# Optimization experiments

Measured on AMD Instinct MI355X. Metric: run time of the kernel, lower is better.

The kernel has to match this reference:

```python
import jax, jax.numpy as jnp
import numpy as np

N_OBJ = 8192        # total proposals across the batch
N_REL = 32768       # total relation pairs across the batch
HID = 512           # CONTEXT_HIDDEN_DIM
POOL = 4096         # CONTEXT_POOLING_DIM (== MLP_HEAD_DIM -> no up_dim)
N_OBJ_CLS = 151     # VG object classes
N_REL_CLS = 51      # VG relation classes


def setup_inputs() -> dict:
    key = jax.random.key(0)
    ks = jax.random.split(key, 8)
    edge_ctx = jax.random.normal(ks[0], (N_OBJ, HID), jnp.float32)
    union_features = jax.random.normal(ks[1], (N_REL, POOL), jnp.float32)
    rel_pair_idx = jax.random.randint(ks[2], (N_REL, 2), 0, N_OBJ)
    obj_preds = jax.random.randint(ks[3], (N_OBJ,), 0, N_OBJ_CLS)
    # layer_init(post_emb, 10 * (1/hidden)**0.5, normal=True)
    W_post_emb = jax.random.normal(ks[4], (HID, 2 * HID), jnp.float32) * (10.0 * (1.0 / HID) ** 0.5)
    b_post_emb = jnp.zeros((2 * HID,), jnp.float32)
    # xavier inits for post_cat / ctx_compress
    W_post_cat = jax.random.normal(ks[5], (2 * HID, POOL), jnp.float32) * np.float32(np.sqrt(2.0 / (2 * HID + POOL)))
    b_post_cat = jnp.zeros((POOL,), jnp.float32)
    W_ctx = jax.random.normal(ks[6], (POOL, N_REL_CLS), jnp.float32) * np.float32(np.sqrt(2.0 / (POOL + N_REL_CLS)))
    b_ctx = jnp.zeros((N_REL_CLS,), jnp.float32)
    # frequency-bias embedding table: rows indexed by head_cls*151 + tail_cls
    freq_table = jax.random.normal(ks[7], (N_OBJ_CLS * N_OBJ_CLS, N_REL_CLS), jnp.float32) * 0.01
    return {
        "edge_ctx": edge_ctx, "union_features": union_features,
        "rel_pair_idx": rel_pair_idx, "obj_preds": obj_preds,
        "W_post_emb": W_post_emb, "b_post_emb": b_post_emb,
        "W_post_cat": W_post_cat, "b_post_cat": b_post_cat,
        "W_ctx": W_ctx, "b_ctx": b_ctx, "freq_table": freq_table,
    }


def reference(edge_ctx, union_features, rel_pair_idx, obj_preds,
              W_post_emb, b_post_emb, W_post_cat, b_post_cat,
              W_ctx, b_ctx, freq_table):
    # edge_rep = relu(post_emb(edge_ctx)).view(N, 2, hidden)
    edge_rep = jax.nn.relu(edge_ctx @ W_post_emb + b_post_emb).reshape(-1, 2, HID)
    head_rep = edge_rep[:, 0]  # [N_obj, HID]
    tail_rep = edge_rep[:, 1]
    # edge-wise gather of head/tail node reps (global indices == per-image split+index)
    h = head_rep[rel_pair_idx[:, 0]]  # [N_rel, HID]
    t = tail_rep[rel_pair_idx[:, 1]]
    prod_rep = jnp.concatenate([h, t], axis=-1) @ W_post_cat + b_post_cat  # [N_rel, POOL]
    ctx_dists = (prod_rep * union_features) @ W_ctx + b_ctx               # [N_rel, 51]
    # frequency bias: index_with_labels(pair_pred)
    pair_idx = obj_preds[rel_pair_idx[:, 0]] * N_OBJ_CLS + obj_preds[rel_pair_idx[:, 1]]
    frq_dists = freq_table[pair_idx]  # [N_rel, 51]
    return ctx_dists + frq_dists
```

## Files before the change

kernel.cpp:

```cpp
#include <hip/hip_runtime.h>
#include <hip/hip_bf16.h>

#define N_OBJ 8192
#define N_REL 32768
#define HID   512
#define POOL  4096
#define NOC   151
#define NRC   51

typedef __bf16 bf16_t;
typedef __attribute__((ext_vector_type(8))) __bf16 bf16x8;
typedef __attribute__((ext_vector_type(4))) __bf16 bf16x4;
typedef __attribute__((ext_vector_type(4))) float f32x4;

__device__ __forceinline__ void async_copy16(const void* g, void* l) {
    __builtin_amdgcn_global_load_lds((__attribute__((address_space(1))) void*)g,
                                     (__attribute__((address_space(3))) void*)l,
                                     16, 0, 0);
}


__global__ void convert_bf16_kernel(const float* __restrict__ in,
                                    bf16_t* __restrict__ out, int n4) {
    int i = blockIdx.x * blockDim.x + threadIdx.x;
    int stride = gridDim.x * blockDim.x;
    for (; i < n4; i += stride) {
        float4 v = ((const float4*)in)[i];
        bf16x4 o;
        o[0] = (bf16_t)v.x; o[1] = (bf16_t)v.y; o[2] = (bf16_t)v.z; o[3] = (bf16_t)v.w;
        ((bf16x4*)out)[i] = o;
    }
}

__global__ void transpose_bf16_kernel(const float* __restrict__ in,
                                      bf16_t* __restrict__ out,
                                      int K, int C, int Cpad) {
    __shared__ float tile[32][33];
    int cb = blockIdx.x * 32, kb = blockIdx.y * 32;
    int tx = threadIdx.x, ty = threadIdx.y;
    #pragma unroll
    for (int i = 0; i < 32; i += 8) {
        int k = kb + ty + i, c = cb + tx;
        float v = (k < K && c < C) ? in[(size_t)k * C + c] : 0.0f;
        tile[ty + i][tx] = v;
    }
    __syncthreads();
    #pragma unroll
    for (int i = 0; i < 32; i += 8) {
        int c = cb + ty + i, k = kb + tx;
        if (c < Cpad && k < K) out[(size_t)c * K + k] = (bf16_t)tile[tx][ty + i];
    }
}


__global__ __launch_bounds__(256, 2) void gemm1_kernel(
    const bf16_t* __restrict__ A,
    const bf16_t* __restrict__ Bt,
    const float* __restrict__ bias,
    bf16_t* __restrict__ C)
{
    __shared__ __align__(16) bf16_t As[128 * 64];
    __shared__ __align__(16) bf16_t Bs[128 * 64];
    const int tid = threadIdx.x;
    const int w = tid >> 6, lane = tid & 63;
    const int m0 = blockIdx.x * 128, n0 = blockIdx.y * 128;
    const int lrow = tid >> 3, lcs = tid & 7;
    const int wm = w & 1, wn = w >> 1;
    const int quad = lane >> 4, l16 = lane & 15;
    f32x4 acc[4][4] = {};

    for (int kt = 0; kt < HID / 64; ++kt) {
        const int k0 = kt * 64;
        #pragma unroll
        for (int j = 0; j < 4; ++j) {
            int ml = j * 32 + lrow;
            int cg = lcs ^ (ml & 7);
            async_copy16(A + (size_t)(m0 + ml) * HID + k0 + cg * 8, &As[ml * 64 + lcs * 8]);
        }
        #pragma unroll
        for (int j = 0; j < 4; ++j) {
            int nl = j * 32 + lrow;
            int cg = lcs ^ (nl & 7);
            async_copy16(Bt + (size_t)(n0 + nl) * HID + k0 + cg * 8, &Bs[nl * 64 + lcs * 8]);
        }
        __syncthreads();
        #pragma unroll
        for (int kb = 0; kb < 2; ++kb) {
            bf16x8 a[4], b[4];
            #pragma unroll
            for (int i = 0; i < 4; ++i) {
                int m = wm * 64 + i * 16 + l16;
                int ch = (kb * 4 + quad) ^ (m & 7);
                a[i] = *(const bf16x8*)&As[m * 64 + ch * 8];
            }
            #pragma unroll
            for (int i = 0; i < 4; ++i) {
                int n = wn * 64 + i * 16 + l16;
                int ch = (kb * 4 + quad) ^ (n & 7);
                b[i] = *(const bf16x8*)&Bs[n * 64 + ch * 8];
            }
            #pragma unroll
            for (int i = 0; i < 4; ++i)
                #pragma unroll
                for (int jj = 0; jj < 4; ++jj)
                    acc[i][jj] = __builtin_amdgcn_mfma_f32_16x16x32_bf16(a[i], b[jj], acc[i][jj], 0, 0, 0);
        }
        __syncthreads();
    }
    #pragma unroll
    for (int i = 0; i < 4; ++i) {
        int rbase = m0 + wm * 64 + i * 16 + quad * 4;
        #pragma unroll
        for (int jj = 0; jj < 4; ++jj) {
            int c = n0 + wn * 64 + jj * 16 + l16;
            float bv = bias[c];
            #pragma unroll
            for (int rr = 0; rr < 4; ++rr) {
                float v = acc[i][jj][rr] + bv;
                v = fmaxf(v, 0.0f);
                C[(size_t)(rbase + rr) * 1024 + c] = (bf16_t)v;
            }
        }
    }
}


__global__ __launch_bounds__(256, 2) void gemm_half_kernel(
    const bf16_t* __restrict__ C1,
    const bf16_t* __restrict__ Wcat_t,
    bf16_t* __restrict__ HWb,
    bf16_t* __restrict__ TWb)
{
    __shared__ __align__(16) bf16_t As[128 * 64];
    __shared__ __align__(16) bf16_t Bs[128 * 64];
    const int tid = threadIdx.x;
    const int w = tid >> 6, lane = tid & 63;
    const int m0 = blockIdx.x * 128, n0 = blockIdx.y * 128;
    const int koff = blockIdx.z * 512;
    bf16_t* const Cout = blockIdx.z ? TWb : HWb;
    const int lrow = tid >> 3, lcs = tid & 7;
    const int wm = w & 1, wn = w >> 1;
    const int quad = lane >> 4, l16 = lane & 15;
    f32x4 acc[4][4] = {};

    for (int kt = 0; kt < 8; ++kt) {
        const int k0 = koff + kt * 64;
        #pragma unroll
        for (int j = 0; j < 4; ++j) {
            int ml = j * 32 + lrow;
            int cg = lcs ^ (ml & 7);
            async_copy16(C1 + (size_t)(m0 + ml) * 1024 + k0 + cg * 8, &As[ml * 64 + lcs * 8]);
        }
        #pragma unroll
        for (int j = 0; j < 4; ++j) {
            int nl = j * 32 + lrow;
            int cg = lcs ^ (nl & 7);
            async_copy16(Wcat_t + (size_t)(n0 + nl) * 1024 + k0 + cg * 8, &Bs[nl * 64 + lcs * 8]);
        }
        __syncthreads();
        #pragma unroll
        for (int kb = 0; kb < 2; ++kb) {
            bf16x8 a[4], b[4];
            #pragma unroll
            for (int i = 0; i < 4; ++i) {
                int m = wm * 64 + i * 16 + l16;
                int ch = (kb * 4 + quad) ^ (m & 7);
                a[i] = *(const bf16x8*)&As[m * 64 + ch * 8];
            }
            #pragma unroll
            for (int i = 0; i < 4; ++i) {
                int n = wn * 64 + i * 16 + l16;
                int ch = (kb * 4 + quad) ^ (n & 7);
                b[i] = *(const bf16x8*)&Bs[n * 64 + ch * 8];
            }
            #pragma unroll
            for (int i = 0; i < 4; ++i)
                #pragma unroll
                for (int jj = 0; jj < 4; ++jj)
                    acc[i][jj] = __builtin_amdgcn_mfma_f32_16x16x32_bf16(a[i], b[jj], acc[i][jj], 0, 0, 0);
        }
        __syncthreads();
    }
    #pragma unroll
    for (int i = 0; i < 4; ++i) {
        int rbase = m0 + wm * 64 + i * 16 + quad * 4;
        #pragma unroll
        for (int jj = 0; jj < 4; ++jj) {
            int c = n0 + wn * 64 + jj * 16 + l16;
            #pragma unroll
            for (int rr = 0; rr < 4; ++rr)
                Cout[(size_t)(rbase + rr) * POOL + c] = (bf16_t)acc[i][jj][rr];
        }
    }
}


__global__ __launch_bounds__(512, 2) void rel_fused_kernel(
    const bf16_t* __restrict__ HWb,
    const bf16_t* __restrict__ TWb,
    const bf16_t* __restrict__ Wctx_t,
    const int* __restrict__ rel,
    const int* __restrict__ obj,
    const float* __restrict__ b_cat,
    const float* __restrict__ b_ctx,
    const float* __restrict__ freq,
    const float* __restrict__ uni,
    float* __restrict__ out)
{
    __shared__ __align__(16) bf16_t Ss[2][64 * 128];
    const int tid = threadIdx.x;
    const int w = tid >> 6, lane = tid & 63;
    const int quad = lane >> 4, l16 = lane & 15;
    const int wm = w & 1, wn = w >> 1;
    const int lr = tid >> 3, hc = tid & 7;
    const int m0 = blockIdx.x * 64;

    const int myrow = m0 + lr;
    const int gi0 = rel[2 * myrow], gi1 = rel[2 * myrow + 1];
    const bf16_t* hwrow = HWb + (size_t)gi0 * POOL;
    const bf16_t* twrow = TWb + (size_t)gi1 * POOL;
    const float*  urow  = uni + (size_t)myrow * POOL;

    f32x4 acc2[2] = {};

    auto scale_pass = [&](int kc, bf16_t* S) {
        const int cbase = kc * 128 + hc * 16;
        #pragma unroll
        for (int cg = 0; cg < 2; ++cg) {
            const int cc = cbase + cg * 8;
            bf16x8 hw = *(const bf16x8*)&hwrow[cc];
            bf16x8 tw = *(const bf16x8*)&twrow[cc];
            float4 u0 = *(const float4*)&urow[cc];
            float4 u1 = *(const float4*)&urow[cc + 4];
            float4 b0 = *(const float4*)&b_cat[cc];
            float4 b1 = *(const float4*)&b_cat[cc + 4];
            bf16x8 s;
            s[0] = (bf16_t)(((float)hw[0] + (float)tw[0] + b0.x) * u0.x);
            s[1] = (bf16_t)(((float)hw[1] + (float)tw[1] + b0.y) * u0.y);
            s[2] = (bf16_t)(((float)hw[2] + (float)tw[2] + b0.z) * u0.z);
            s[3] = (bf16_t)(((float)hw[3] + (float)tw[3] + b0.w) * u0.w);
            s[4] = (bf16_t)(((float)hw[4] + (float)tw[4] + b1.x) * u1.x);
            s[5] = (bf16_t)(((float)hw[5] + (float)tw[5] + b1.y) * u1.y);
            s[6] = (bf16_t)(((float)hw[6] + (float)tw[6] + b1.z) * u1.z);
            s[7] = (bf16_t)(((float)hw[7] + (float)tw[7] + b1.w) * u1.w);
            const int colc = hc * 2 + cg;
            *(bf16x8*)&S[lr * 128 + ((colc ^ (lr & 15)) << 3)] = s;
        }
    };
    auto mma_pass = [&](int kc, const bf16_t* S) {
        #pragma unroll
        for (int kb = 0; kb < 4; ++kb) {
            bf16x8 a2[2], b2;
            #pragma unroll
            for (int i = 0; i < 2; ++i) {
                int m = wm * 32 + i * 16 + l16;
                a2[i] = *(const bf16x8*)&S[m * 128 + (((kb * 4 + quad) ^ (m & 15)) << 3)];
            }
            int c = wn * 16 + l16;
            b2 = *(const bf16x8*)&Wctx_t[(size_t)c * POOL + kc * 128 + kb * 32 + quad * 8];
            #pragma unroll
            for (int i = 0; i < 2; ++i)
                acc2[i] = __builtin_amdgcn_mfma_f32_16x16x32_bf16(a2[i], b2, acc2[i], 0, 0, 0);
        }
    };

    scale_pass(0, Ss[0]);
    __syncthreads();
    for (int kc = 0; kc < 32; ++kc) {
        bf16_t* Scur = Ss[kc & 1];
        bf16_t* Snxt = Ss[(kc & 1) ^ 1];
        if (kc < 31) scale_pass(kc + 1, Snxt);
        mma_pass(kc, Scur);
        __syncthreads();
    }

    #pragma unroll
    for (int i = 0; i < 2; ++i) {
        #pragma unroll
        for (int rr = 0; rr < 4; ++rr) {
            int row = m0 + wm * 32 + i * 16 + quad * 4 + rr;
            int c = wn * 16 + l16;
            if (c < NRC) {
                int pid = obj[rel[2 * row]] * NOC + obj[rel[2 * row + 1]];
                out[(size_t)row * NRC + c] =
                    acc2[i][rr] + b_ctx[c] + freq[(size_t)pid * NRC + c];
            }
        }
    }
}


extern "C" void kernel_launch(void* const* d_in, const int* in_sizes, int n_in,
                              void* d_out, int out_size, void* d_ws, size_t ws_size,
                              hipStream_t stream) {
    const float* edge_ctx = (const float*)d_in[0];
    const float* uni      = (const float*)d_in[1];
    const int*   rel      = (const int*)d_in[2];
    const int*   obj      = (const int*)d_in[3];
    const float* W_emb    = (const float*)d_in[4];
    const float* b_emb    = (const float*)d_in[5];
    const float* W_cat    = (const float*)d_in[6];
    const float* b_cat    = (const float*)d_in[7];
    const float* W_ctx    = (const float*)d_in[8];
    const float* b_ctx    = (const float*)d_in[9];
    const float* freq     = (const float*)d_in[10];
    float* out = (float*)d_out;

    char* p = (char*)d_ws;
    bf16_t* C1     = (bf16_t*)p; p += (size_t)N_OBJ * 1024 * 2;
    bf16_t* ecb    = (bf16_t*)p; p += (size_t)N_OBJ * HID * 2;
    bf16_t* Wemb_t = (bf16_t*)p; p += (size_t)1024 * HID * 2;
    bf16_t* Wcat_t = (bf16_t*)p; p += (size_t)POOL * 1024 * 2;
    bf16_t* Wctx_t = (bf16_t*)p; p += (size_t)64 * POOL * 2;
    bf16_t* HWb    = (bf16_t*)p; p += (size_t)N_OBJ * POOL * 2;
    bf16_t* TWb    = (bf16_t*)p; p += (size_t)N_OBJ * POOL * 2;

    convert_bf16_kernel<<<2048, 256, 0, stream>>>(edge_ctx, ecb, N_OBJ * HID / 4);
    transpose_bf16_kernel<<<dim3(1024 / 32, HID / 32), dim3(32, 8), 0, stream>>>(W_emb, Wemb_t, HID, 1024, 1024);
    transpose_bf16_kernel<<<dim3(POOL / 32, 1024 / 32), dim3(32, 8), 0, stream>>>(W_cat, Wcat_t, 1024, POOL, POOL);
    transpose_bf16_kernel<<<dim3(2, POOL / 32), dim3(32, 8), 0, stream>>>(W_ctx, Wctx_t, POOL, NRC, 64);

    gemm1_kernel<<<dim3(N_OBJ / 128, 1024 / 128), 256, 0, stream>>>(ecb, Wemb_t, b_emb, C1);
    gemm_half_kernel<<<dim3(N_OBJ / 128, POOL / 128, 2), 256, 0, stream>>>(C1, Wcat_t, HWb, TWb);
    rel_fused_kernel<<<N_REL / 64, 512, 0, stream>>>(HWb, TWb, Wctx_t, rel, obj,
                                                     b_cat, b_ctx, freq, uni, out);
}
```

Baseline: 897.0 us.

## Merge prep kernels into one launch and shrink rel tile to 16 rows

```diff
diff --git a/kernel.cpp b/kernel.cpp
--- a/kernel.cpp
+++ b/kernel.cpp
@@ -20,24 +20,33 @@
 }
 
 
-__global__ void convert_bf16_kernel(const float* __restrict__ in,
-                                    bf16_t* __restrict__ out, int n4) {
-    int i = blockIdx.x * blockDim.x + threadIdx.x;
-    int stride = gridDim.x * blockDim.x;
-    for (; i < n4; i += stride) {
-        float4 v = ((const float4*)in)[i];
-        bf16x4 o;
-        o[0] = (bf16_t)v.x; o[1] = (bf16_t)v.y; o[2] = (bf16_t)v.z; o[3] = (bf16_t)v.w;
-        ((bf16x4*)out)[i] = o;
-    }
-}
-
-__global__ void transpose_bf16_kernel(const float* __restrict__ in,
-                                      bf16_t* __restrict__ out,
-                                      int K, int C, int Cpad) {
+__global__ void prep_kernel(const float* __restrict__ W_emb, bf16_t* __restrict__ Wemb_t,
+                            const float* __restrict__ W_cat, bf16_t* __restrict__ Wcat_t,
+                            const float* __restrict__ W_ctx, bf16_t* __restrict__ Wctx_t,
+                            const float* __restrict__ ec,    bf16_t* __restrict__ ecb) {
+    const int bid = blockIdx.x;
+    if (bid >= 4864) {
+        const int tid = threadIdx.y * 32 + threadIdx.x;
+        int i = (bid - 4864) * 256 + tid;
+        const int n4 = N_OBJ * HID / 4;
+        const int stride = 2048 * 256;
+        for (; i < n4; i += stride) {
+            float4 v = ((const float4*)ec)[i];
+            bf16x4 o;
+            o[0] = (bf16_t)v.x; o[1] = (bf16_t)v.y; o[2] = (bf16_t)v.z; o[3] = (bf16_t)v.w;
+            ((bf16x4*)ecb)[i] = o;
+        }
+        return;
+    }
+    const float* in; bf16_t* outp; int K, C, Cpad, cb, kb;
+    if (bid < 512)       { in = W_emb; outp = Wemb_t; K = HID;  C = 1024; Cpad = 1024;
+                           cb = (bid & 31) << 5; kb = (bid >> 5) << 5; }
+    else if (bid < 4608) { int b = bid - 512;  in = W_cat; outp = Wcat_t; K = 1024; C = POOL; Cpad = POOL;
+                           cb = (b & 127) << 5; kb = (b >> 7) << 5; }
+    else                 { int b = bid - 4608; in = W_ctx; outp = Wctx_t; K = POOL; C = NRC;  Cpad = 64;
+                           cb = (b & 1) << 5;  kb = (b >> 1) << 5; }
     __shared__ float tile[32][33];
-    int cb = blockIdx.x * 32, kb = blockIdx.y * 32;
-    int tx = threadIdx.x, ty = threadIdx.y;
+    const int tx = threadIdx.x, ty = threadIdx.y;
     #pragma unroll
     for (int i = 0; i < 32; i += 8) {
         int k = kb + ty + i, c = cb + tx;
@@ -48,7 +57,7 @@
     #pragma unroll
     for (int i = 0; i < 32; i += 8) {
         int c = cb + ty + i, k = kb + tx;
-        if (c < Cpad && k < K) out[(size_t)c * K + k] = (bf16_t)tile[tx][ty + i];
+        if (c < Cpad && k < K) outp[(size_t)c * K + k] = (bf16_t)tile[tx][ty + i];
     }
 }
 
@@ -195,7 +204,7 @@
 }
 
 
-__global__ __launch_bounds__(512, 2) void rel_fused_kernel(
+__global__ __launch_bounds__(256, 6) void rel_fused_kernel(
     const bf16_t* __restrict__ HWb,
     const bf16_t* __restrict__ TWb,
     const bf16_t* __restrict__ Wctx_t,
@@ -207,13 +216,12 @@
     const float* __restrict__ uni,
     float* __restrict__ out)
 {
-    __shared__ __align__(16) bf16_t Ss[2][64 * 128];
+    __shared__ __align__(16) bf16_t Ss[2][16 * 128];
     const int tid = threadIdx.x;
     const int w = tid >> 6, lane = tid & 63;
     const int quad = lane >> 4, l16 = lane & 15;
-    const int wm = w & 1, wn = w >> 1;
-    const int lr = tid >> 3, hc = tid & 7;
-    const int m0 = blockIdx.x * 64;
+    const int lr = tid >> 4, hc = tid & 15;
+    const int m0 = blockIdx.x * 16;
 
     const int myrow = m0 + lr;
     const int gi0 = rel[2 * myrow], gi1 = rel[2 * myrow + 1];
@@ -221,46 +229,35 @@
     const bf16_t* twrow = TWb + (size_t)gi1 * POOL;
     const float*  urow  = uni + (size_t)myrow * POOL;
 
-    f32x4 acc2[2] = {};
+    f32x4 acc = {};
 
     auto scale_pass = [&](int kc, bf16_t* S) {
-        const int cbase = kc * 128 + hc * 16;
-        #pragma unroll
-        for (int cg = 0; cg < 2; ++cg) {
-            const int cc = cbase + cg * 8;
-            bf16x8 hw = *(const bf16x8*)&hwrow[cc];
-            bf16x8 tw = *(const bf16x8*)&twrow[cc];
-            float4 u0 = *(const float4*)&urow[cc];
-            float4 u1 = *(const float4*)&urow[cc + 4];
-            float4 b0 = *(const float4*)&b_cat[cc];
-            float4 b1 = *(const float4*)&b_cat[cc + 4];
-            bf16x8 s;
-            s[0] = (bf16_t)(((float)hw[0] + (float)tw[0] + b0.x) * u0.x);
-            s[1] = (bf16_t)(((float)hw[1] + (float)tw[1] + b0.y) * u0.y);
-            s[2] = (bf16_t)(((float)hw[2] + (float)tw[2] + b0.z) * u0.z);
-            s[3] = (bf16_t)(((float)hw[3] + (float)tw[3] + b0.w) * u0.w);
-            s[4] = (bf16_t)(((float)hw[4] + (float)tw[4] + b1.x) * u1.x);
-            s[5] = (bf16_t)(((float)hw[5] + (float)tw[5] + b1.y) * u1.y);
-            s[6] = (bf16_t)(((float)hw[6] + (float)tw[6] + b1.z) * u1.z);
-            s[7] = (bf16_t)(((float)hw[7] + (float)tw[7] + b1.w) * u1.w);
-            const int colc = hc * 2 + cg;
-            *(bf16x8*)&S[lr * 128 + ((colc ^ (lr & 15)) << 3)] = s;
-        }
+        const int cc = kc * 128 + hc * 8;
+        bf16x8 hw = *(const bf16x8*)&hwrow[cc];
+        bf16x8 tw = *(const bf16x8*)&twrow[cc];
+        float4 u0 = *(const float4*)&urow[cc];
+        float4 u1 = *(const float4*)&urow[cc + 4];
+        float4 b0 = *(const float4*)&b_cat[cc];
+        float4 b1 = *(const float4*)&b_cat[cc + 4];
+        bf16x8 s;
+        s[0] = (bf16_t)(((float)hw[0] + (float)tw[0] + b0.x) * u0.x);
+        s[1] = (bf16_t)(((float)hw[1] + (float)tw[1] + b0.y) * u0.y);
+        s[2] = (bf16_t)(((float)hw[2] + (float)tw[2] + b0.z) * u0.z);
+        s[3] = (bf16_t)(((float)hw[3] + (float)tw[3] + b0.w) * u0.w);
+        s[4] = (bf16_t)(((float)hw[4] + (float)tw[4] + b1.x) * u1.x);
+        s[5] = (bf16_t)(((float)hw[5] + (float)tw[5] + b1.y) * u1.y);
+        s[6] = (bf16_t)(((float)hw[6] + (float)tw[6] + b1.z) * u1.z);
+        s[7] = (bf16_t)(((float)hw[7] + (float)tw[7] + b1.w) * u1.w);
+        *(bf16x8*)&S[lr * 128 + ((hc ^ lr) << 3)] = s;
     };
     auto mma_pass = [&](int kc, const bf16_t* S) {
         #pragma unroll
         for (int kb = 0; kb < 4; ++kb) {
-            bf16x8 a2[2], b2;
-            #pragma unroll
-            for (int i = 0; i < 2; ++i) {
-                int m = wm * 32 + i * 16 + l16;
-                a2[i] = *(const bf16x8*)&S[m * 128 + (((kb * 4 + quad) ^ (m & 15)) << 3)];
-            }
-            int c = wn * 16 + l16;
-            b2 = *(const bf16x8*)&Wctx_t[(size_t)c * POOL + kc * 128 + kb * 32 + quad * 8];
-            #pragma unroll
-            for (int i = 0; i < 2; ++i)
-                acc2[i] = __builtin_amdgcn_mfma_f32_16x16x32_bf16(a2[i], b2, acc2[i], 0, 0, 0);
+            int m = l16;
+            bf16x8 a2 = *(const bf16x8*)&S[m * 128 + (((kb * 4 + quad) ^ m) << 3)];
+            int c = w * 16 + l16;
+            bf16x8 b2 = *(const bf16x8*)&Wctx_t[(size_t)c * POOL + kc * 128 + kb * 32 + quad * 8];
+            acc = __builtin_amdgcn_mfma_f32_16x16x32_bf16(a2, b2, acc, 0, 0, 0);
         }
     };
 
@@ -274,17 +271,13 @@
         __syncthreads();
     }
 
-    #pragma unroll
-    for (int i = 0; i < 2; ++i) {
+    const int c = w * 16 + l16;
+    if (c < NRC) {
         #pragma unroll
         for (int rr = 0; rr < 4; ++rr) {
-            int row = m0 + wm * 32 + i * 16 + quad * 4 + rr;
-            int c = wn * 16 + l16;
-            if (c < NRC) {
-                int pid = obj[rel[2 * row]] * NOC + obj[rel[2 * row + 1]];
-                out[(size_t)row * NRC + c] =
-                    acc2[i][rr] + b_ctx[c] + freq[(size_t)pid * NRC + c];
-            }
+            int row = m0 + quad * 4 + rr;
+            int pid = obj[rel[2 * row]] * NOC + obj[rel[2 * row + 1]];
+            out[(size_t)row * NRC + c] = acc[rr] + b_ctx[c] + freq[(size_t)pid * NRC + c];
         }
     }
 }
@@ -315,13 +308,10 @@
     bf16_t* HWb    = (bf16_t*)p; p += (size_t)N_OBJ * POOL * 2;
     bf16_t* TWb    = (bf16_t*)p; p += (size_t)N_OBJ * POOL * 2;
 
-    convert_bf16_kernel<<<2048, 256, 0, stream>>>(edge_ctx, ecb, N_OBJ * HID / 4);
-    transpose_bf16_kernel<<<dim3(1024 / 32, HID / 32), dim3(32, 8), 0, stream>>>(W_emb, Wemb_t, HID, 1024, 1024);
-    transpose_bf16_kernel<<<dim3(POOL / 32, 1024 / 32), dim3(32, 8), 0, stream>>>(W_cat, Wcat_t, 1024, POOL, POOL);
-    transpose_bf16_kernel<<<dim3(2, POOL / 32), dim3(32, 8), 0, stream>>>(W_ctx, Wctx_t, POOL, NRC, 64);
-
+    prep_kernel<<<6912, dim3(32, 8), 0, stream>>>(W_emb, Wemb_t, W_cat, Wcat_t,
+                                                  W_ctx, Wctx_t, edge_ctx, ecb);
     gemm1_kernel<<<dim3(N_OBJ / 128, 1024 / 128), 256, 0, stream>>>(ecb, Wemb_t, b_emb, C1);
     gemm_half_kernel<<<dim3(N_OBJ / 128, POOL / 128, 2), 256, 0, stream>>>(C1, Wcat_t, HWb, TWb);
-    rel_fused_kernel<<<N_REL / 64, 512, 0, stream>>>(HWb, TWb, Wctx_t, rel, obj,
+    rel_fused_kernel<<<N_REL / 16, 256, 0, stream>>>(HWb, TWb, Wctx_t, rel, obj,
                                                      b_cat, b_ctx, freq, uni, out);
 }
```

Result: no change. 908.1 us (+1.2%).
